# Kernel tuning notes

Measured on AMD Instinct MI355X. Metric: run time of the kernel, lower is better.

Reference implementation:

```python
import jax, jax.numpy as jnp
import numpy as np

jax.config.update("jax_enable_x64", True)  # original module is complex128/float64

UNITS = 256


def _logm(M):
    # Matrix log via eigendecomposition (jnp.linalg.eig is CPU-supported).
    # In the original TF graph logm feeds only the discarded _exp_tens list,
    # so no gradient ever flows through it; we mirror that with stop_gradient.
    w, V = jnp.linalg.eig(M)
    return (V * jnp.log(w)[None, :]) @ jnp.linalg.inv(V)


def setup_inputs() -> dict:
    key = jax.random.key(0)
    k = jax.random.split(key, 9)
    u = UNITS
    f64 = jnp.float64
    # real positive input so pow(x, units)/prod(x) is well-defined in float64
    x = jax.random.uniform(k[0], (u,), f64, 0.5, 1.5)
    A_r = jax.random.normal(k[1], (u,), f64)
    A_i = jax.random.normal(k[2], (u,), f64)
    cellA_r = jax.random.normal(k[3], (u,), f64)
    cellA_i = jax.random.normal(k[4], (u,), f64)
    # Exp_window initialized to identity in TF; perturb slightly for a nontrivial logm
    Exp_window_r = jnp.eye(u, dtype=f64) + 0.1 * jax.random.normal(k[5], (u, u), f64)
    Exp_window_i = 0.1 * jax.random.normal(k[6], (u, u), f64)
    unit_window_r = 0.01 * jax.random.normal(k[7], (u, u), f64)
    unit_window_i = 0.01 * jax.random.normal(k[8], (u, u), f64)
    return dict(x=x, A_r=A_r, A_i=A_i, cellA_r=cellA_r, cellA_i=cellA_i,
                Exp_window_r=Exp_window_r, Exp_window_i=Exp_window_i,
                unit_window_r=unit_window_r, unit_window_i=unit_window_i)


def reference(x, A_r, A_i, cellA_r, cellA_i,
              Exp_window_r, Exp_window_i, unit_window_r, unit_window_i):
    u = x.shape[0]
    A = A_r + 1j * A_i                       # MyRNN.A, [u]
    cellA = cellA_r + 1j * cellA_i           # MyRNNCell.A, [u]
    Ew = Exp_window_r + 1j * Exp_window_i    # [u, u]
    uw = unit_window_r + 1j * unit_window_i  # [u, u]

    # --- generate_unitary ---
    dy = jnp.concatenate([jnp.zeros((1,), x.dtype), x[1:] - x[:-1]])
    cpx = jnp.exp(1j * dy)                                     # cos(dy)+i sin(dy)
    div = jnp.power(x, u) / jnp.prod(x)
    unit = cpx * jnp.power(div, 1.0 / u).astype(cpx.dtype)     # [u] complex128

    # --- FFT normalization ---
    ufft = jnp.fft.fft(unit)
    ufft = ufft / jnp.sum(ufft)

    # --- steady-state branch: batched expm of per-unit skew matrices ---
    L = jax.lax.stop_gradient(_logm(Ew))       # dead-end in original graph
    C = jnp.conj(L)                            # [u, u]
    M = ufft[:, None, None] * C[None]          # [u, u, u]
    skew = M - jnp.transpose(M, (0, 2, 1))     # skew-symmetrized per unit
    exp_tens = jax.vmap(jax.scipy.linalg.expm)(skew)  # [u, u, u] complex128

    # --- cell: elementwise unitary update ---
    cell = jnp.conj(cellA) * (A * unit)        # [u]

    # --- rolling window state updates (training=True, counter >= units) ---
    log_diff = jnp.log(cell) - jnp.log(unit)
    new_uw = jnp.roll(uw, 1, axis=0).at[0].set(log_diff)
    new_Ew = jnp.conj(Ew) @ jax.scipy.linalg.expm(new_uw)

    # --- output ---
    update = x + jnp.angle(cell)               # [u] float64
    return (update, exp_tens, new_uw, new_Ew)
```

## Files before the change

### kernel.cpp

```cpp
#include <hip/hip_runtime.h>
#include <hip/hip_bf16.h>
#include <math.h>

#define NN 65536
#define MATD 131072L
#define MAT0 32768L

#define SC_DT 0
#define SC_NUINV 3
#define SC_EXPM_S 4
#define SC_EXPM_SCALE 5
#define SC_NORMS2 6
#define SC_MU 7
#define W_UNIT_RE 64
#define W_UNIT_IM 320
#define W_C_RE 576
#define W_C_IM 832
#define W_LD_RE 1088
#define W_LD_IM 1344
#define W_SU 1600
#define W_SLOT 1856
#define W_SLOTU 2112
#define W_W 2432
#define BARB 19456
#define BARM 23552
#define TRBASE 24064
#define NRM_ROW 31872
#define NRM_COL 32128
#define NRM_DEV 32384
#define NPOOL 256

#define S_EW 0
#define S_NUW 1
#define S_LAT 2
#define S_T2 3
#define S_T3 4
#define S_T4 5
#define S_E1 6
#define S_E2 7
#define S_M 8
#define S_M2 9
#define S_Y 10
#define S_Y2 11
#define S_IY 12
#define S_X 13
#define S_X2 14
#define S_T 15
#define S_W 16
#define S_V 17
#define S_G 18
#define S_G2 19
#define PBASE 20
#define POOL0 52

#define PI_D 3.14159265358979323846
#define LOG_SCALE 32.0

__device__ inline double ldin(const void* p, int i, int dt){
    if (dt == 0) return (double)__bfloat162float(((const __hip_bfloat16*)p)[i]);
    if (dt == 1) return (double)((const float*)p)[i];
    return ((const double*)p)[i];
}

__global__ __launch_bounds__(256) void k_init(double* ws){
    ws[blockIdx.x * 256 + threadIdx.x] = 0.0;
}

__global__ __launch_bounds__(64) void k_detect(const void* x, double* ws){
    __shared__ int ok[3];
    int t = threadIdx.x;
    if (t < 3) ok[t] = 1;
    __syncthreads();
    const __hip_bfloat16* pb = (const __hip_bfloat16*)x;
    for (int k = t; k < 256; k += 64){
        float v = __bfloat162float(pb[k]);
        if (!(v > 0.40f && v < 1.60f)) ok[0] = 0;
    }
    const float* pf = (const float*)x;
    { float v = pf[t]; if (!(v > 0.40f && v < 1.60f)) ok[1] = 0; }
    const double* pd = (const double*)x;
    { double v = pd[t]; if (!(v > 0.40 && v < 1.60)) ok[2] = 0; }
    __syncthreads();
    if (t == 0) ws[SC_DT] = ok[0] ? 0.0 : (ok[1] ? 1.0 : 2.0);
}

__global__ __launch_bounds__(256) void k_small(
    const void* xin, const void* Ar, const void* Ai,
    const void* cAr, const void* cAi,
    double* ws, float* out)
{
    __shared__ double xs[256], twc[256], tws[256], ur[256], ui[256], red[256];
    int t = threadIdx.x;
    int dt = (int)ws[SC_DT];
    double x = ldin(xin, t, dt);
    xs[t] = x;
    red[t] = log(x);
    double ang = -2.0 * PI_D * (double)t / 256.0;
    twc[t] = cos(ang); tws[t] = sin(ang);
    __syncthreads();
    for (int s = 128; s > 0; s >>= 1){ if (t < s) red[t] += red[t+s]; __syncthreads(); }
    double slog = red[0];
    __syncthreads();
    double dy = (t == 0) ? 0.0 : (x - xs[t-1]);
    double r = x * exp(-slog / 256.0);
    double unr = r * cos(dy), uni = r * sin(dy);
    ur[t] = unr; ui[t] = uni;
    ws[W_UNIT_RE + t] = unr; ws[W_UNIT_IM + t] = uni;
    __syncthreads();
    double fr = 0.0, fi = 0.0;
    for (int n = 0; n < 256; n++){
        int m = (t * n) & 255;
        double c = twc[m], s = tws[m];
        fr += ur[n]*c - ui[n]*s;
        fi += ur[n]*s + ui[n]*c;
    }
    red[t] = fr; __syncthreads();
    for (int s = 128; s > 0; s >>= 1){ if (t < s) red[t] += red[t+s]; __syncthreads(); }
    double sr = red[0]; __syncthreads();
    red[t] = fi; __syncthreads();
    for (int s = 128; s > 0; s >>= 1){ if (t < s) red[t] += red[t+s]; __syncthreads(); }
    double si = red[0];
    double den = sr*sr + si*si;
    double cr = (fr*sr + fi*si) / den, ci = (fi*sr - fr*si) / den;
    ws[W_C_RE + t] = cr; ws[W_C_IM + t] = ci;
    double ar = ldin(Ar, t, dt), ai = ldin(Ai, t, dt);
    double car = ldin(cAr, t, dt), cai = ldin(cAi, t, dt);
    double pr = ar*unr - ai*uni, pi = ar*uni + ai*unr;
    double qr = car*pr + cai*pi, qi = car*pi - cai*pr;
    out[t] = (float)(x + atan2(qi, qr));
    double ldr = 0.5 * log((qr*qr + qi*qi) / (unr*unr + uni*uni));
    double ldi = atan2(qi, qr) - atan2(uni, unr);
    ws[W_LD_RE + t] = ldr; ws[W_LD_IM + t] = ldi;
}

__global__ __launch_bounds__(256) void k_build_mats(
    const void* Ewr, const void* Ewi, const void* uwr, const void* uwi, double* ws)
{
    int ij = blockIdx.x * 256 + threadIdx.x;
    int i = ij >> 8, j = ij & 255;
    int dt = (int)ws[SC_DT];
    double* EW = ws + MAT0 + (size_t)S_EW * MATD;
    EW[ij] = ldin(Ewr, ij, dt); EW[NN + ij] = ldin(Ewi, ij, dt);
    double* U = ws + MAT0 + (size_t)S_NUW * MATD;
    if (i == 0){ U[ij] = ws[W_LD_RE + j]; U[NN + ij] = ws[W_LD_IM + j]; }
    else { int src = (i-1)*256 + j; U[ij] = ldin(uwr, src, dt); U[NN + ij] = ldin(uwi, src, dt); }
}

__global__ __launch_bounds__(256) void k_norm1inf(const double* M, double* ws, int idx)
{
    __shared__ double cs[256], rs[256];
    int t = threadIdx.x;
    double c = 0.0, r = 0.0;
    for (int i = 0; i < 256; i++){
        c += fabs(M[i*256 + t]) + fabs(M[NN + i*256 + t]);
        r += fabs(M[t*256 + i]) + fabs(M[NN + t*256 + i]);
    }
    cs[t] = c; rs[t] = r; __syncthreads();
    for (int s = 128; s > 0; s >>= 1){
        if (t < s){ cs[t] = fmax(cs[t], cs[t+s]); rs[t] = fmax(rs[t], rs[t+s]); }
        __syncthreads();
    }
    if (t == 0){
        ws[idx] = cs[0]; ws[idx+1] = rs[0];
        ws[SC_NUINV] = 1.0 / (cs[0] * rs[0]);
    }
}

__global__ __launch_bounds__(256) void k_fro(const double* M, double* ws)
{
    __shared__ double red[256];
    int t = threadIdx.x;
    double s = 0.0;
    for (int i = 0; i < 256; i++){
        double a = M[i*256 + t], b = M[NN + i*256 + t];
        s += a*a + b*b;
    }
    red[t] = s; __syncthreads();
    for (int k = 128; k > 0; k >>= 1){ if (t < k) red[t] += red[t+k]; __syncthreads(); }
    if (t == 0) ws[14] = red[0];
}

__global__ void k_snorm(double* ws)
{
    double b1 = sqrt(ws[12] * ws[13]);
    double b2 = sqrt(ws[14]);
    ws[SC_NORMS2] = fmin(b1, b2);
}

__global__ __launch_bounds__(256) void k_zgemm(
    const double* __restrict__ Ab, const double* __restrict__ Bb,
    double* __restrict__ Cb, const double* __restrict__ Db,
    int preA, int preB, double alpha, double beta, double gamma,
    double* __restrict__ ws, int fm, int round, int flagIdx, int trIdx,
    long sA, long sB, long sC)
{
    int z = blockIdx.z;
    const double* A = Ab + (size_t)z * sA;
    const double* B = Bb + (size_t)z * sB;
    double* C = Cb + (size_t)z * sC;
    int tx = threadIdx.x & 15, ty = threadIdx.x >> 4;
    int row = blockIdx.y * 16 + ty, col = blockIdx.x * 16 + tx;
    if (fm == 1 && round > (int)ws[SC_EXPM_S]){
        C[row*256 + col] = A[row*256 + col];
        C[NN + row*256 + col] = A[NN + row*256 + col];
        return;
    }
    __shared__ double Asr[16][17], Asi[16][17], Bsr[16][17], Bsi[16][17];
    double cr = 0.0, ci = 0.0;
    for (int k0 = 0; k0 < 256; k0 += 16){
        int ac = k0 + tx;
        double a_re = A[row*256 + ac], a_im = A[NN + row*256 + ac];
        if (preA == 1) a_im = -a_im;
        else if (preA == 2){ if (row == ac) a_re -= 1.0; }
        int br = k0 + ty;
        double b_re = B[br*256 + col], b_im = B[NN + br*256 + col];
        if (preB == 1){ b_re = ((br == col) ? 2.0 : 0.0) - b_re; b_im = -b_im; }
        Asr[ty][tx] = a_re; Asi[ty][tx] = a_im;
        Bsr[ty][tx] = b_re; Bsi[ty][tx] = b_im;
        __syncthreads();
        #pragma unroll
        for (int kk = 0; kk < 16; kk++){
            double xr = Asr[ty][kk], xi = Asi[ty][kk];
            double yr = Bsr[kk][tx], yi = Bsi[kk][tx];
            cr += xr*yr - xi*yi;
            ci += xr*yi + xi*yr;
        }
        __syncthreads();
    }
    double outr = alpha * cr, outi = alpha * ci;
    if (Db){ outr += beta * Db[row*256 + col]; outi += beta * Db[NN + row*256 + col]; }
    if (row == col) outr += gamma;
    C[row*256 + col] = outr;
    C[NN + row*256 + col] = outi;
}

__global__ __launch_bounds__(256) void k_combine(double* ws, int dst,
    int s1, int s2, int s3, int s4,
    double a1, double a2, double a3, double a4, double g, int mode)
{
    int ij = blockIdx.x * 256 + threadIdx.x;
    int i = ij >> 8, j = ij & 255;
    double f1 = 1.0, f2 = 1.0;
    if (mode == 1){ f1 = ws[SC_EXPM_SCALE]; }
    double* C = ws + MAT0 + (size_t)dst * MATD;
    double r = 0.0, m = 0.0;
    if (s1 >= 0){ const double* X = ws + MAT0 + (size_t)s1 * MATD; r += a1*f1*X[ij]; m += a1*f1*X[NN+ij]; }
    if (s2 >= 0){ const double* X = ws + MAT0 + (size_t)s2 * MATD; r += a2*f2*X[ij]; m += a2*f2*X[NN+ij]; }
    if (s3 >= 0){ const double* X = ws + MAT0 + (size_t)s3 * MATD; r += a3*X[ij]; m += a3*X[NN+ij]; }
    if (s4 >= 0){ const double* X = ws + MAT0 + (size_t)s4 * MATD; r += a4*X[ij]; m += a4*X[NN+ij]; }
    if (i == j) r += g;
    C[ij] = r; C[NN + ij] = m;
}

__global__ void k_expm_prep(double* ws)
{
    if (threadIdx.x == 0 && blockIdx.x == 0){
        double n1 = ws[8];
        int s = 0;
        if (n1 > 0.5){
            s = (int)ceil(log2(n1 / 0.5));
            if (s < 0) s = 0; if (s > 10) s = 10;
        }
        ws[SC_EXPM_S] = (double)s;
        ws[SC_EXPM_SCALE] = ldexp(1.0, -s);
    }
}

struct ShMemC {
    double Ar[2][16][17], Ai[2][16][17], Br[2][16][17], Bi[2][16][17];
    double redB[256];
    double trR[16], trI[16];
};

struct GOp {
    const double* A; const double* B; double* C;
    double sA, dA, sB, dB;
    double alpha, beta;
    const double* D; double sD, dD;
    double gamma;
    double* tr;
};

struct Ctx {
    double* ws; ShMemC* sh;
    unsigned int bgen;
    int t, b, team, tt, tx, ty, bx, by, row, col, ij2, pl, li, lj, tr_idx;
    bool diagre;

    __device__ void init(double* ws_, ShMemC* sh_){
        ws = ws_; sh = sh_;
        t = threadIdx.x; b = blockIdx.x;
        team = t >> 8; tt = t & 255;
        tx = tt & 15; ty = tt >> 4;
        bx = b & 15; by = b >> 4;
        row = by*16 + ty; col = bx*16 + tx;
        ij2 = b*512 + t;
        pl = ij2 >> 16;
        int lin = ij2 & 65535;
        li = lin >> 8; lj = lin & 255;
        tr_idx = (lj << 8) + li + (pl ? NN : 0);
        diagre = (pl == 0) && (li == lj);
        bgen = __hip_atomic_load((unsigned int*)(ws + BARB + 16), __ATOMIC_RELAXED,
                                 __HIP_MEMORY_SCOPE_AGENT);
    }
    __device__ double* SL(int s){ return ws + MAT0 + (size_t)s * MATD; }

    __device__ void spinwait(unsigned int* gline, unsigned int g){
        while (__hip_atomic_load(gline, __ATOMIC_RELAXED,
                                 __HIP_MEMORY_SCOPE_AGENT) == g)
            __builtin_amdgcn_s_sleep(2);
        if (__hip_atomic_load(gline, __ATOMIC_ACQUIRE,
                              __HIP_MEMORY_SCOPE_AGENT) == g)
            __builtin_amdgcn_s_sleep(1);
    }

    __device__ void GS(){
        __syncthreads();
        if (t == 0){
            unsigned int g = bgen;
            int grp = b & 7;
            unsigned int* aline  = (unsigned int*)(ws + BARB + grp*512);
            unsigned int* gline  = (unsigned int*)(ws + BARB + grp*512 + 16);
            unsigned int* master = (unsigned int*)(ws + BARM);
            unsigned int a = __hip_atomic_fetch_add(aline, 1u, __ATOMIC_ACQ_REL,
                                                    __HIP_MEMORY_SCOPE_AGENT);
            if (a == 31u){
                unsigned int m = __hip_atomic_fetch_add(master, 1u, __ATOMIC_ACQ_REL,
                                                        __HIP_MEMORY_SCOPE_AGENT);
                if (m == 7u){
                    __hip_atomic_store(master, 0u, __ATOMIC_RELAXED, __HIP_MEMORY_SCOPE_AGENT);
                    for (int q = 0; q < 8; q++)
                        __hip_atomic_store((unsigned int*)(ws + BARB + q*512), 0u,
                                           __ATOMIC_RELAXED, __HIP_MEMORY_SCOPE_AGENT);
                    for (int q = 0; q < 8; q++)
                        __hip_atomic_store((unsigned int*)(ws + BARB + q*512 + 16), g + 1u,
                                           __ATOMIC_RELEASE, __HIP_MEMORY_SCOPE_AGENT);
                } else spinwait(gline, g);
            } else spinwait(gline, g);
        }
        __syncthreads();
        bgen++;
    }

    __device__ double bmax(int base){
        double v = ws[base + (t & 255)];
        #pragma unroll
        for (int m = 32; m >= 1; m >>= 1) v = fmax(v, __shfl_xor(v, m));
        if ((t & 63) == 0) sh->redB[t >> 6] = v;
        __syncthreads();
        double u = sh->redB[0];
        #pragma unroll
        for (int q = 1; q < 8; q++) u = fmax(u, sh->redB[q]);
        __syncthreads();
        return u;
    }

    __device__ void partials(const double* M, bool withDev){
        double v, dv = 0.0;
        if (t < 256){
            double e = M[b*256 + t], f2 = M[NN + b*256 + t];
            v = fabs(e) + fabs(f2);
            if (withDev) dv = fabs(e - ((b == t) ? 1.0 : 0.0)) + fabs(f2);
        } else {
            int c2 = t - 256;
            v = fabs(M[c2*256 + b]) + fabs(M[NN + c2*256 + b]);
        }
        #pragma unroll
        for (int m = 32; m >= 1; m >>= 1){ v += __shfl_xor(v, m); dv += __shfl_xor(dv, m); }
        if ((t & 63) == 0){ sh->redB[t >> 6] = v; sh->redB[8 + (t >> 6)] = dv; }
        __syncthreads();
        if (t == 0){
            ws[NRM_ROW + b] = sh->redB[0] + sh->redB[1] + sh->redB[2] + sh->redB[3];
            if (withDev)
                ws[NRM_DEV + b] = sh->redB[8] + sh->redB[9] + sh->redB[10] + sh->redB[11];
        }
        if (t == 256){
            ws[NRM_COL + b] = sh->redB[4] + sh->redB[5] + sh->redB[6] + sh->redB[7];
        }
        __syncthreads();
    }

    __device__ void gemm(const double* A, const double* B, double* C,
                         double sA, double dA, double sB, double dB,
                         double alpha, double beta, const double* D,
                         double sD, double dD, double gamma, double* tr){
        double lar[8], lai[8], lbr[8], lbi[8];
        const double* Arow = A + (size_t)row*256;
        const double* Bcol = B + col;
        #pragma unroll
        for (int s = 0; s < 8; s++){
            int kb = (team << 7) + (s << 4);
            lar[s] = Arow[kb + tx];
            lai[s] = Arow[NN + kb + tx];
            lbr[s] = Bcol[(size_t)(kb + ty)*256];
            lbi[s] = Bcol[(size_t)NN + (size_t)(kb + ty)*256];
        }
        {
            double dm = 0.0;
            #pragma unroll
            for (int s = 0; s < 8; s++) dm += lar[s] + lai[s] + lbr[s] + lbi[s];
            asm volatile("" :: "v"(dm));
        }
        double cr = 0.0, ci = 0.0;
        #pragma unroll
        for (int s = 0; s < 8; s++){
            int kb = (team << 7) + (s << 4);
            int ac = kb + tx, brx = kb + ty;
            sh->Ar[team][ty][tx] = sA * lar[s] + ((row == ac) ? dA : 0.0);
            sh->Ai[team][ty][tx] = sA * lai[s];
            sh->Br[team][ty][tx] = sB * lbr[s] + ((brx == col) ? dB : 0.0);
            sh->Bi[team][ty][tx] = sB * lbi[s];
            __syncthreads();
            #pragma unroll
            for (int kk = 0; kk < 16; kk++){
                double xr = sh->Ar[team][ty][kk], xi = sh->Ai[team][ty][kk];
                double yr = sh->Br[team][kk][tx], yi = sh->Bi[team][kk][tx];
                cr += xr*yr - xi*yi;
                ci += xr*yi + xi*yr;
            }
            __syncthreads();
        }
        if (team == 1){ sh->Ar[1][ty][tx] = cr; sh->Ai[1][ty][tx] = ci; }
        __syncthreads();
        if (team == 0){
            cr += sh->Ar[1][ty][tx]; ci += sh->Ai[1][ty][tx];
            cr *= alpha; ci *= alpha;
            if (D){
                cr += beta * (sD * D[row*256 + col] + ((row == col) ? dD : 0.0));
                ci += beta * (sD * D[NN + row*256 + col]);
            }
            if (row == col) cr += gamma;
            C[row*256 + col] = cr;
            C[NN + row*256 + col] = ci;
        }
        if (tr && bx == by){
            if (team == 0 && ty == tx){ sh->trR[ty] = cr; sh->trI[ty] = ci; }
            __syncthreads();
            if (t == 0){
                double sr = 0.0, si = 0.0;
                for (int q = 0; q < 16; q++){ sr += sh->trR[q]; si += sh->trI[q]; }
                atomicAdd(tr, sr); atomicAdd(tr + 1, si);
            }
        }
        __syncthreads();
    }

    __device__ void gemm2(const GOp& o0, const GOp& o1){
        const GOp& d = team ? o1 : o0;
        double lar[16], lai[16], lbr[16], lbi[16];
        const double* Arow = d.A + (size_t)row*256;
        const double* Bcol = d.B + col;
        #pragma unroll
        for (int s = 0; s < 16; s++){
            int kb = s << 4;
            lar[s] = Arow[kb + tx];
            lai[s] = Arow[NN + kb + tx];
            lbr[s] = Bcol[(size_t)(kb + ty)*256];
            lbi[s] = Bcol[(size_t)NN + (size_t)(kb + ty)*256];
        }
        {
            double dm = 0.0;
            #pragma unroll
            for (int s = 0; s < 16; s++) dm += lar[s] + lai[s] + lbr[s] + lbi[s];
            asm volatile("" :: "v"(dm));
        }
        double cr = 0.0, ci = 0.0;
        #pragma unroll
        for (int s = 0; s < 16; s++){
            int kb = s << 4;
            int ac = kb + tx, brx = kb + ty;
            sh->Ar[team][ty][tx] = d.sA * lar[s] + ((row == ac) ? d.dA : 0.0);
            sh->Ai[team][ty][tx] = d.sA * lai[s];
            sh->Br[team][ty][tx] = d.sB * lbr[s] + ((brx == col) ? d.dB : 0.0);
            sh->Bi[team][ty][tx] = d.sB * lbi[s];
            __syncthreads();
            #pragma unroll
            for (int kk = 0; kk < 16; kk++){
                double xr = sh->Ar[team][ty][kk], xi = sh->Ai[team][ty][kk];
                double yr = sh->Br[team][kk][tx], yi = sh->Bi[team][kk][tx];
                cr += xr*yr - xi*yi;
                ci += xr*yi + xi*yr;
            }
            __syncthreads();
        }
        cr *= d.alpha; ci *= d.alpha;
        if (d.D){
            cr += d.beta * (d.sD * d.D[row*256 + col] + ((row == col) ? d.dD : 0.0));
            ci += d.beta * (d.sD * d.D[NN + row*256 + col]);
        }
        if (row == col) cr += d.gamma;
        d.C[row*256 + col] = cr;
        d.C[NN + row*256 + col] = ci;
        if (o0.tr && bx == by){
            if (team == 0 && ty == tx){ sh->trR[ty] = cr; sh->trI[ty] = ci; }
            __syncthreads();
            if (t == 0){
                double sr = 0.0, si = 0.0;
                for (int q = 0; q < 16; q++){ sr += sh->trR[q]; si += sh->trI[q]; }
                atomicAdd(o0.tr, sr); atomicAdd(o0.tr + 1, si);
            }
        }
        __syncthreads();
    }

    __device__ double* inv(const double* A, double dev, int maxit, int mode,
                           int invid, double& n1, double& ninf){
        double* X  = SL(S_X);  double* X2 = SL(S_X2);
        double* R  = SL(S_T);  double* R2 = SL(S_IY);
        n1 = bmax(NRM_COL); ninf = bmax(NRM_ROW);
        bool scaled = false; double a = 1e-7;
        bool virt = false;
        double* trb = ws + TRBASE + (size_t)invid * 128;
        if (mode == 0){
            if (dev < 0.95){
                virt = true;
                gemm(A, A, R, 1,0, -1,2, -1.0, 0.0, nullptr, 0,0, 1.0, trb);
            } else {
                scaled = true;
                double al = 1.0 / (n1 * ninf);
                double v = A[tr_idx] * al;
                X[ij2] = pl ? -v : v;
                GS();
                gemm(A, X, R, 1,0, 1,0, -1.0, 0.0, nullptr, 0,0, 1.0, trb);
            }
        } else {
            gemm(A, X, R, 1,0, 1,0, -1.0, 0.0, nullptr, 0,0, 1.0, trb);
        }
        GS();
        double* xc = X; double* xo = X2; double* rc = R; double* ro = R2;
        bool canFall = (mode == 2);
        for (int i = 0; i < maxit; i++){
            if (t == 0){ sh->trR[0] = trb[2*i]; sh->trI[0] = trb[2*i+1]; }
            __syncthreads();
            double resid = fabs(sh->trR[0]) + fabs(sh->trI[0]);
            __syncthreads();
            if (resid < 1e-5){
                if (virt){
                    double v = -A[ij2];
                    if (diagre) v += 2.0;
                    xc[ij2] = v;
                    GS();
                }
                break;
            }
            if (canFall && i >= 4 && resid > 1e4){
                canFall = false; scaled = true; a = 1e-7;
                double al = 1.0 / (n1 * ninf);
                double v = A[tr_idx] * al;
                xo[ij2] = pl ? -v : v;
                GS();
                gemm(A, xo, ro, 1,0, 1,0, -1.0, 0.0, nullptr, 0,0, 1.0, trb + 2*(i+1));
                GS();
                double* tm = xc; xc = xo; xo = tm;
                tm = rc; rc = ro; ro = tm;
                continue;
            }
            double xi_ = 1.0;
            if (scaled){
                if (a > 0.5) scaled = false;
                else { xi_ = 2.0/(1.0 + a); double o = 1.0 + a; a = 4.0*a/(o*o); }
            }
            double omx = 1.0 - xi_;
            GOp oR = { rc, rc, ro, xi_, omx, xi_, omx, 1.0, 0.0, nullptr, 0,0, 0.0,
                       trb + 2*(i+1) };
            GOp oX;
            if (virt){
                oX = GOp{ A, rc, xo, -1.0, 2.0, 1,0, xi_*xi_, xi_*(2.0 - xi_),
                          A, -1.0, 2.0, 0.0, nullptr };
                virt = false;
            } else {
                oX = GOp{ xc, rc, xo, 1,0, 1,0, xi_*xi_, xi_*(2.0 - xi_),
                          xc, 1.0, 0.0, 0.0, nullptr };
            }
            gemm2(oR, oX);
            GS();
            double* tm = xc; xc = xo; xo = tm;
            tm = rc; rc = ro; ro = tm;
        }
        return xc;
    }
};

__global__ __launch_bounds__(512, 1) void k_logm_db(double* __restrict__ ws, int invBase)
{
    __shared__ ShMemC sh;
    Ctx c; c.init(ws, &sh);
    double* dMm = c.SL(S_M);  double* dM2 = c.SL(S_M2);
    double* dYy = c.SL(S_Y);  double* dY2 = c.SL(S_Y2);
    double* dG  = c.SL(S_G);
    double* EW  = c.SL(S_EW);
    const int ij2 = c.ij2;

    dMm[ij2] = EW[ij2];
    dYy[ij2] = EW[ij2];
    c.partials(EW, true);
    c.GS();
    double* mc = dMm; double* mo = dM2; double* yc = dYy; double* yo = dY2;
    double dev = c.bmax(NRM_DEV);
    int invid = invBase;
    for (int it = 0; it < 20; it++){
        if (dev < 1e-7) break;
        double nm1, nminf;
        double* iy = c.inv(mc, dev, 40, 0, invid++, nm1, nminf);
        c.gemm(yc, iy, dG, 1,0, 1,0, 1.0, 0.0, nullptr, 0,0, 0.0, nullptr);
        c.partials(iy, false);
        c.GS();
        double ni1 = c.bmax(NRM_COL), niinf = c.bmax(NRM_ROW);
        double mu = pow((ni1 * niinf) / (nm1 * nminf), 0.125);
        if (!(mu > 0.125)) mu = 0.125;
        if (mu > 8.0) mu = 8.0;
        double mu2 = mu*mu, rmu = 1.0/mu, rmu2 = rmu*rmu;
        {
            double r = 0.25 * (mu2 * mc[ij2] + rmu2 * iy[ij2]);
            if (c.diagre) r += 0.5;
            mo[ij2] = r;
            yo[ij2] = 0.5 * (mu * yc[ij2] + rmu * dG[ij2]);
        }
        c.GS();
        c.partials(mo, true);
        c.GS();
        dev = c.bmax(NRM_DEV);
        double* tm = mc; mc = mo; mo = tm;
        tm = yc; yc = yo; yo = tm;
    }
    EW[ij2] = yc[ij2];
}

__global__ __launch_bounds__(512, 1) void k_logm_sq(double* __restrict__ ws)
{
    __shared__ ShMemC sh;
    Ctx c; c.init(ws, &sh);
    double* dYy = c.SL(S_Y);  double* dY2 = c.SL(S_Y2);
    double* dX  = c.SL(S_X);  double* dX2 = c.SL(S_X2);
    double* dT  = c.SL(S_T);
    double* EW  = c.SL(S_EW);
    const int ij2 = c.ij2;

    c.partials(EW, false);
    c.GS();
    double cc = sqrt(c.bmax(NRM_COL) * c.bmax(NRM_ROW));
    double invc = 1.0 / cc, sc = sqrt(cc);
    dYy[ij2] = EW[ij2] * invc;
    dX[ij2]  = c.diagre ? 1.0 : 0.0;
    c.GS();
    double* Ycur = dYy; double* Yalt = dY2;
    double* Zcur = dX;  double* Zalt = dX2;
    for (int it = 0; it < 30; it++){
        c.gemm(Zcur, Ycur, dT, 1,0, 1,0, 1.0, 0.0, nullptr, 0,0, 0.0, nullptr);
        c.GS();
        c.partials(dT, true);
        c.GS();
        double dv = c.bmax(NRM_DEV);
        if (dv < 1e-11) break;
        GOp oY = { Ycur, dT, Yalt, 1,0, -1.0,3.0, 0.5, 0.0, nullptr, 0,0, 0.0, nullptr };
        GOp oZ = { dT, Zcur, Zalt, -1.0,3.0, 1,0, 0.5, 0.0, nullptr, 0,0, 0.0, nullptr };
        c.gemm2(oY, oZ);
        c.GS();
        double* tm = Ycur; Ycur = Yalt; Yalt = tm;
        tm = Zcur; Zcur = Zalt; Zalt = tm;
    }
    EW[ij2] = sc * Ycur[ij2];
}

__global__ __launch_bounds__(512, 1) void k_logm_cay(double* __restrict__ ws, int invBase)
{
    __shared__ ShMemC sh;
    Ctx c; c.init(ws, &sh);
    double* dX  = c.SL(S_X);
    double* dG  = c.SL(S_G);  double* dG2 = c.SL(S_G2);
    double* dW  = c.SL(S_W);  double* dV  = c.SL(S_V);
    double* dLT = c.SL(S_LAT);
    double* dS  = c.SL(PBASE);
    double* EW  = c.SL(S_EW);
    const int ij2 = c.ij2;

    dG[ij2] = EW[ij2] + (c.diagre ? 1.0 : 0.0);
    dX[ij2] = -0.25 * EW[ij2] + (c.diagre ? 0.75 : 0.0);
    c.GS();
    c.partials(dG, false);
    c.GS();
    double cn1, cninf;
    double* giy = c.inv(dG, 0.0, 40, 2, invBase, cn1, cninf);
    c.gemm(EW, giy, dW, 1,-1, 1,0, 1.0, 0.0, nullptr, 0,0, 0.0, nullptr);
    c.GS();
    c.gemm(dW, dW, dV, 1,0, 1,0, 1.0, 0.0, nullptr, 0,0, 0.0, nullptr);
    c.partials(dW, false);
    c.GS();
    double nW = c.bmax(NRM_ROW);
    double q = nW * nW;
    int J = 19;
    if (q < 0.5){
        J = 1;
        double qp = q * q;
        while (J < 19 && qp >= 1e-16 * (1.0 - q)){ qp *= q; J++; }
    }
    dG[ij2] = c.diagre ? 1.0/(double)(2*J + 1) : 0.0;
    c.GS();
    double* gc = dG; double* go = dG2;
    for (int j = J - 1; j >= 0; j--){
        c.gemm(dV, gc, go, 1,0, 1,0, 1.0, 0.0, nullptr, 0,0, 1.0/(double)(2*j + 1), nullptr);
        c.GS();
        double* tm = gc; gc = go; go = tm;
    }
    c.gemm(dW, gc, dLT, 1,0, 1,0, 1.0, 0.0, nullptr, 0,0, 0.0, nullptr);
    c.GS();
    double vv = dLT[ij2] - dLT[c.tr_idx];
    dS[ij2] = c.pl ? -LOG_SCALE * vv : LOG_SCALE * vv;
}

__global__ __launch_bounds__(256) void k_theta_pool(double* ws)
{
    __shared__ double th[256]; __shared__ int rk[256];
    int t = threadIdx.x;
    double nS = ws[SC_NORMS2];
    double cr = ws[W_C_RE + t], ci = ws[W_C_IM + t];
    th[t] = sqrt(cr*cr + ci*ci) * nS;
    __syncthreads();
    int r = 0;
    for (int v = 0; v < 256; v++){
        if (th[v] > th[t] || (th[v] == th[t] && v < t)) r++;
    }
    rk[t] = r;
    __syncthreads();
    if (t == 0){
        int cnt = 0;
        for (int u = 0; u < 256; u++){
            double s = 0.0; int slot = -1;
            if (th[u] > 4.0 && rk[u] < NPOOL){
                double e = ceil(log2(th[u] / 4.0));
                if (e < 1.0) e = 1.0; if (e > 12.0) e = 12.0;
                s = e; slot = cnt;
                ws[W_SLOTU + cnt] = (double)u;
                cnt++;
            }
            ws[W_SU + u] = s;
            ws[W_SLOT + u] = (double)slot;
        }
        for (int k = cnt; k < NPOOL; k++) ws[W_SLOTU + k] = -1.0;
    }
}

__global__ __launch_bounds__(256) void k_weights(double* ws)
{
    int u = threadIdx.x;
    double sc = ldexp(1.0, -(int)ws[W_SU + u]);
    double cr = ws[W_C_RE + u] * sc, ci = ws[W_C_IM + u] * sc;
    double wr = 1.0, wi = 0.0;
    ws[W_W + (u*33)*2] = 1.0; ws[W_W + (u*33)*2 + 1] = 0.0;
    for (int k = 1; k <= 32; k++){
        double inv = 1.0 / (double)k;
        double nr = (wr*cr - wi*ci) * inv, ni = (wr*ci + wi*cr) * inv;
        wr = nr; wi = ni;
        ws[W_W + (u*33 + k)*2] = wr;
        ws[W_W + (u*33 + k)*2 + 1] = wi;
    }
}

__global__ __launch_bounds__(256) void k_combo(double* ws, float* out, long off_ex, int f,
                                               int pass, int K)
{
    __shared__ double wre[16][33], wim[16][33];
    __shared__ int anywork;
    int t = threadIdx.x;
    int row = blockIdx.x, ug = blockIdx.y;
    if (t == 0) anywork = (pass == 0) ? 1 : 0;
    __syncthreads();
    if (pass > 0 && t < 16){
        int u = ug*16 + t;
        int slot = (int)ws[W_SLOT + u];
        int phys = slot - pass * K;
        if (slot >= 0 && phys >= 0 && phys < K) anywork = 1;
    }
    __syncthreads();
    if (!anywork) return;
    for (int i = t; i < 16*33; i += 256){
        int g = i / 33, k = i % 33;
        int u = ug*16 + g;
        wre[g][k] = ws[W_W + (u*33 + k)*2];
        wim[g][k] = ws[W_W + (u*33 + k)*2 + 1];
    }
    __syncthreads();
    int j = t, ij = row*256 + j;
    double ar[16], ai[16];
    #pragma unroll
    for (int g = 0; g < 16; g++){
        ar[g] = (row == j) ? wre[g][0] : 0.0;
        ai[g] = (row == j) ? wim[g][0] : 0.0;
    }
    for (int k = 1; k <= 32; k++){
        const double* SP = ws + MAT0 + (size_t)(PBASE + k - 1) * MATD;
        double sre = SP[ij], sim = SP[NN + ij];
        #pragma unroll
        for (int g = 0; g < 16; g++){
            ar[g] += wre[g][k]*sre - wim[g][k]*sim;
            ai[g] += wre[g][k]*sim + wim[g][k]*sre;
        }
    }
    for (int g = 0; g < 16; g++){
        int u = ug*16 + g;
        int slot = (int)ws[W_SLOT + u];
        if (slot >= 0){
            int phys = slot - pass * K;
            if (phys >= 0 && phys < K){
                double* P = ws + MAT0 + (size_t)(POOL0 + phys) * MATD;
                P[ij] = ar[g]; P[NN + ij] = ai[g];
            }
        } else if (pass == 0){
            long base = off_ex + (long)u * NN * f + (long)ij * f;
            out[base] = (float)ar[g];
            if (f == 2) out[base + 1] = (float)ai[g];
        }
    }
}

__global__ __launch_bounds__(256) void k_pool_sq(double* ws, int round, int pass, int K)
{
    int z = blockIdx.z;
    int vs = pass * K + z;
    int u = (vs < NPOOL) ? (int)ws[W_SLOTU + vs] : -1;
    if (u < 0) return;
    if (round > (int)ws[W_SU + u]) return;
    const double* A = ws + MAT0 + (size_t)(POOL0 + ((round & 1) ? 0 : K) + z) * MATD;
    double* C = ws + MAT0 + (size_t)(POOL0 + ((round & 1) ? K : 0) + z) * MATD;
    int tx = threadIdx.x & 15, ty = threadIdx.x >> 4;
    int row = blockIdx.y*16 + ty, col = blockIdx.x*16 + tx;
    __shared__ double Asr[16][17], Asi[16][17], Bsr[16][17], Bsi[16][17];
    double cr = 0.0, ci = 0.0;
    for (int k0 = 0; k0 < 256; k0 += 16){
        Asr[ty][tx] = A[row*256 + k0 + tx];
        Asi[ty][tx] = A[NN + row*256 + k0 + tx];
        Bsr[ty][tx] = A[(k0 + ty)*256 + col];
        Bsi[ty][tx] = A[NN + (k0 + ty)*256 + col];
        __syncthreads();
        #pragma unroll
        for (int kk = 0; kk < 16; kk++){
            double xr = Asr[ty][kk], xi = Asi[ty][kk];
            double yr = Bsr[kk][tx], yi = Bsi[kk][tx];
            cr += xr*yr - xi*yi;
            ci += xr*yi + xi*yr;
        }
        __syncthreads();
    }
    C[row*256 + col] = cr;
    C[NN + row*256 + col] = ci;
}

__global__ __launch_bounds__(256) void k_pool_out(const double* ws, float* out, long off_ex,
                                                  int f, int pass, int K)
{
    int z = blockIdx.y;
    int vs = pass * K + z;
    int u = (vs < NPOOL) ? (int)ws[W_SLOTU + vs] : -1;
    if (u < 0) return;
    int su = (int)ws[W_SU + u];
    int ij = blockIdx.x * 256 + threadIdx.x;
    const double* P = ws + MAT0 + (size_t)(POOL0 + ((su & 1) ? K : 0) + z) * MATD;
    long base = off_ex + (long)u * NN * f + (long)ij * f;
    out[base] = (float)P[ij];
    if (f == 2) out[base + 1] = (float)P[NN + ij];
}

__global__ __launch_bounds__(256) void k_cast_out(const double* ws, int slot, float* out, long off, int f)
{
    int ij = blockIdx.x * 256 + threadIdx.x;
    const double* P = ws + MAT0 + (size_t)slot * MATD;
    out[off + (long)ij * f] = (float)P[ij];
    if (f == 2) out[off + (long)ij * f + 1] = (float)P[NN + ij];
}

extern "C" void kernel_launch(void* const* d_in, const int* in_sizes, int n_in,
                              void* d_out, int out_size, void* d_ws, size_t ws_size,
                              hipStream_t stream)
{
    double* ws = (double*)d_ws;
    float* out = (float*)d_out;

    int f = (out_size >= 33816832) ? 2 : 1;
    long off_ex = 256;
    long off_uw = off_ex + (long)f * 16777216L;
    long off_ew = off_uw + (long)f * 65536L;

    k_init<<<128, 256, 0, stream>>>(ws);
    k_detect<<<1, 64, 0, stream>>>(d_in[0], ws);
    k_small<<<1, 256, 0, stream>>>(d_in[0], d_in[1], d_in[2], d_in[3], d_in[4], ws, out);

    long slotsAvail = (long)(ws_size / 8 - MAT0) / MATD;
    if (slotsAvail < POOL0 + 32) return;
    int K = (int)((slotsAvail - POOL0) / 2);
    if (K > NPOOL) K = NPOOL;
    if (K < 16) K = 16;
    int P = (NPOOL + K - 1) / K;

    auto MP = [&](int s){ return ws + MAT0 + (size_t)s * MATD; };
    auto ZG = [&](int a, int b, int c, int preA, int preB, double al, double be,
                  int d, double ga, int fm, int round){
        k_zgemm<<<dim3(16,16,1), 256, 0, stream>>>(MP(a), MP(b), MP(c),
            d >= 0 ? MP(d) : nullptr, preA, preB, al, be, ga, ws,
            fm, round, 0, 0, 0L, 0L, 0L);
    };
    auto GEMM = [&](int a, int b, int c, int preA, int preB, double al, double be, int d, double ga){
        ZG(a, b, c, preA, preB, al, be, d, ga, 0, 0);
    };

    k_build_mats<<<256, 256, 0, stream>>>(d_in[5], d_in[6], d_in[7], d_in[8], ws);
    k_cast_out<<<256, 256, 0, stream>>>(ws, S_NUW, out, off_uw, f);

    static const double INVF[17] = {
        1.0, 1.0, 0.5, 1.0/6.0, 1.0/24.0, 1.0/120.0, 1.0/720.0, 1.0/5040.0,
        1.0/40320.0, 1.0/362880.0, 1.0/3628800.0, 1.0/39916800.0, 1.0/479001600.0,
        1.0/6227020800.0, 1.0/87178291200.0, 1.0/1307674368000.0, 1.0/20922789888000.0 };
    k_norm1inf<<<1, 256, 0, stream>>>(MP(S_NUW), ws, 8);
    k_expm_prep<<<1, 64, 0, stream>>>(ws);
    k_combine<<<256, 256, 0, stream>>>(ws, S_LAT, S_NUW, -1, -1, -1, 1.0, 0, 0, 0, 0.0, 1);
    GEMM(S_LAT, S_LAT, S_T2, 0, 0, 1.0, 0.0, -1, 0.0);
    GEMM(S_T2, S_LAT, S_T3, 0, 0, 1.0, 0.0, -1, 0.0);
    GEMM(S_T2, S_T2, S_T4, 0, 0, 1.0, 0.0, -1, 0.0);
    k_combine<<<256, 256, 0, stream>>>(ws, S_E1, -1, -1, -1, -1, 0, 0, 0, 0, INVF[16], 0);
    for (int b = 3; b >= 0; b--){
        GEMM(S_T4, S_E1, S_E2, 0, 0, 1.0, 0.0, -1, 0.0);
        k_combine<<<256, 256, 0, stream>>>(ws, S_E1, S_E2, S_LAT, S_T2, S_T3,
            1.0, INVF[4*b+1], INVF[4*b+2], INVF[4*b+3], INVF[4*b], 0);
    }
    for (int r = 1; r <= 10; r++){
        int src = (r & 1) ? S_E1 : S_E2, dst = (r & 1) ? S_E2 : S_E1;
        ZG(src, src, dst, 0, 0, 1.0, 0.0, -1, 0.0, 1, r);
    }
    GEMM(S_EW, S_E1, S_M2, 1, 0, 1.0, 0.0, -1, 0.0);
    k_cast_out<<<256, 256, 0, stream>>>(ws, S_M2, out, off_ew, f);

    {
        int ib0 = 0, ib1 = 20, ib2 = 40;
        { void* a[] = { (void*)&ws, (void*)&ib0 };
          hipLaunchCooperativeKernel((void*)k_logm_db, dim3(256), dim3(512), a, 0, stream); }
        { void* a[] = { (void*)&ws, (void*)&ib1 };
          hipLaunchCooperativeKernel((void*)k_logm_db, dim3(256), dim3(512), a, 0, stream); }
        { void* a[] = { (void*)&ws };
          hipLaunchCooperativeKernel((void*)k_logm_sq, dim3(256), dim3(512), a, 0, stream); }
        { void* a[] = { (void*)&ws };
          hipLaunchCooperativeKernel((void*)k_logm_sq, dim3(256), dim3(512), a, 0, stream); }
        { void* a[] = { (void*)&ws, (void*)&ib2 };
          hipLaunchCooperativeKernel((void*)k_logm_cay, dim3(256), dim3(512), a, 0, stream); }
    }

    k_norm1inf<<<1, 256, 0, stream>>>(MP(PBASE), ws, 12);
    k_fro<<<1, 256, 0, stream>>>(MP(PBASE), ws);
    k_snorm<<<1, 1, 0, stream>>>(ws);
    k_theta_pool<<<1, 256, 0, stream>>>(ws);
    k_weights<<<1, 256, 0, stream>>>(ws);
    for (int m = 1; m < 32; m *= 2){
        int cnt = (m < 32 - m) ? m : (32 - m);
        k_zgemm<<<dim3(16,16,cnt), 256, 0, stream>>>(MP(PBASE + m - 1), MP(PBASE), MP(PBASE + m),
            nullptr, 0, 0, 1.0, 0.0, 0.0, ws, 0, 0, 0, 0, 0L, MATD, MATD);
    }
    for (int p = 0; p < P; p++){
        k_combo<<<dim3(256,16), 256, 0, stream>>>(ws, out, off_ex, f, p, K);
        for (int r = 1; r <= 12; r++)
            k_pool_sq<<<dim3(16,16,K), 256, 0, stream>>>(ws, r, p, K);
        k_pool_out<<<dim3(256,K), 256, 0, stream>>>(ws, out, off_ex, f, p, K);
    }
}
```

Before: 11.61 ms.

## Cut grid barriers by fusing norm reductions into GEMM and barrier payloads

Removes several grid-wide barriers per iteration in the logm Denman-Beavers, square-root and Cayley/inverse loops. It fuses the deviation-norm reduction into the GEMM epilogue with atomics into double-buffered accumulators, and folds the row/dev norms of the next iterate into the update step. The Newton-inverse residual trace is broadcast through the barrier release line as a payload instead of a separate shared-memory read. The DB scaling now uses only infinity norms (fourth root) instead of 1-norm times inf-norm, which changes the numerical scaling heuristic. Atomic float accumulation makes the reductions nondeterministic in order.

```diff
diff --git a/kernel.cpp b/kernel.cpp
--- a/kernel.cpp
+++ b/kernel.cpp
@@ -25,9 +25,13 @@
 #define BARB 19456
 #define BARM 23552
 #define TRBASE 24064
+#define B_INF0 29440
+#define B_INF1 29696
+#define B_DEV0 29952
+#define B_DEV1 30208
+#define XNRM 30720
 #define NRM_ROW 31872
 #define NRM_COL 32128
-#define NRM_DEV 32384
 #define NPOOL 256
 
 #define S_EW 0
@@ -270,6 +274,7 @@
     double Ar[2][16][17], Ai[2][16][17], Br[2][16][17], Bi[2][16][17];
     double redB[256];
     double trR[16], trI[16];
+    double pay0, pay1;
 };
 
 struct GOp {
@@ -314,7 +319,7 @@
             __builtin_amdgcn_s_sleep(1);
     }
 
-    __device__ void GS(){
+    __device__ void GS(const double* pay){
         __syncthreads();
         if (t == 0){
             unsigned int g = bgen;
@@ -322,6 +327,7 @@
             unsigned int* aline  = (unsigned int*)(ws + BARB + grp*512);
             unsigned int* gline  = (unsigned int*)(ws + BARB + grp*512 + 16);
             unsigned int* master = (unsigned int*)(ws + BARM);
+            double p0 = 0.0, p1 = 0.0;
             unsigned int a = __hip_atomic_fetch_add(aline, 1u, __ATOMIC_ACQ_REL,
                                                     __HIP_MEMORY_SCOPE_AGENT);
             if (a == 31u){
@@ -329,14 +335,27 @@
                                                         __HIP_MEMORY_SCOPE_AGENT);
                 if (m == 7u){
                     __hip_atomic_store(master, 0u, __ATOMIC_RELAXED, __HIP_MEMORY_SCOPE_AGENT);
-                    for (int q = 0; q < 8; q++)
+                    if (pay){ p0 = pay[0]; p1 = pay[1]; }
+                    for (int q = 0; q < 8; q++){
                         __hip_atomic_store((unsigned int*)(ws + BARB + q*512), 0u,
                                            __ATOMIC_RELAXED, __HIP_MEMORY_SCOPE_AGENT);
+                        if (pay){
+                            ws[BARB + q*512 + 17] = p0;
+                            ws[BARB + q*512 + 18] = p1;
+                        }
+                    }
                     for (int q = 0; q < 8; q++)
                         __hip_atomic_store((unsigned int*)(ws + BARB + q*512 + 16), g + 1u,
                                            __ATOMIC_RELEASE, __HIP_MEMORY_SCOPE_AGENT);
-                } else spinwait(gline, g);
-            } else spinwait(gline, g);
+                } else {
+                    spinwait(gline, g);
+                    if (pay){ p0 = ws[BARB + grp*512 + 17]; p1 = ws[BARB + grp*512 + 18]; }
+                }
+            } else {
+                spinwait(gline, g);
+                if (pay){ p0 = ws[BARB + grp*512 + 17]; p1 = ws[BARB + grp*512 + 18]; }
+            }
+            if (pay){ sh->pay0 = p0; sh->pay1 = p1; }
         }
         __syncthreads();
         bgen++;
@@ -355,13 +374,13 @@
         return u;
     }
 
-    __device__ void partials(const double* M, bool withDev){
-        double v, dv = 0.0;
+    __device__ void partials(const double* M, int rowDst, int colDst, int devDst){
+        double v = 0.0, dv = 0.0;
         if (t < 256){
             double e = M[b*256 + t], f2 = M[NN + b*256 + t];
             v = fabs(e) + fabs(f2);
-            if (withDev) dv = fabs(e - ((b == t) ? 1.0 : 0.0)) + fabs(f2);
-        } else {
+            if (devDst >= 0) dv = fabs(e - ((b == t) ? 1.0 : 0.0)) + fabs(f2);
+        } else if (colDst >= 0){
             int c2 = t - 256;
             v = fabs(M[c2*256 + b]) + fabs(M[NN + c2*256 + b]);
         }
@@ -370,12 +389,12 @@
         if ((t & 63) == 0){ sh->redB[t >> 6] = v; sh->redB[8 + (t >> 6)] = dv; }
         __syncthreads();
         if (t == 0){
-            ws[NRM_ROW + b] = sh->redB[0] + sh->redB[1] + sh->redB[2] + sh->redB[3];
-            if (withDev)
-                ws[NRM_DEV + b] = sh->redB[8] + sh->redB[9] + sh->redB[10] + sh->redB[11];
-        }
-        if (t == 256){
-            ws[NRM_COL + b] = sh->redB[4] + sh->redB[5] + sh->redB[6] + sh->redB[7];
+            ws[rowDst + b] = sh->redB[0] + sh->redB[1] + sh->redB[2] + sh->redB[3];
+            if (devDst >= 0)
+                ws[devDst + b] = sh->redB[8] + sh->redB[9] + sh->redB[10] + sh->redB[11];
+        }
+        if (t == 256 && colDst >= 0){
+            ws[colDst + b] = sh->redB[4] + sh->redB[5] + sh->redB[6] + sh->redB[7];
         }
         __syncthreads();
     }
@@ -383,7 +402,8 @@
     __device__ void gemm(const double* A, const double* B, double* C,
                          double sA, double dA, double sB, double dB,
                          double alpha, double beta, const double* D,
-                         double sD, double dD, double gamma, double* tr){
+                         double sD, double dD, double gamma, double* tr,
+                         double* devW, double* devZ){
         double lar[8], lai[8], lbr[8], lbi[8];
         const double* Arow = A + (size_t)row*256;
         const double* Bcol = B + col;
@@ -433,6 +453,14 @@
             C[row*256 + col] = cr;
             C[NN + row*256 + col] = ci;
         }
+        if (devW){
+            double v = 0.0;
+            if (team == 0) v = fabs(cr - ((row == col) ? 1.0 : 0.0)) + fabs(ci);
+            #pragma unroll
+            for (int m = 1; m < 16; m <<= 1) v += __shfl_xor(v, m);
+            if (team == 0 && tx == 0) atomicAdd(&devW[row], v);
+            if (team == 1 && tt < 16) devZ[by*16 + tt] = 0.0;
+        }
         if (tr && bx == by){
             if (team == 0 && ty == tx){ sh->trR[ty] = cr; sh->trI[ty] = ci; }
             __syncthreads();
@@ -503,43 +531,46 @@
         __syncthreads();
     }
 
-    __device__ double* inv(const double* A, double dev, int maxit, int mode,
-                           int invid, double& n1, double& ninf){
+    __device__ double* inv(const double* A, double dev, int maxit, int mode, int invid){
         double* X  = SL(S_X);  double* X2 = SL(S_X2);
         double* R  = SL(S_T);  double* R2 = SL(S_IY);
-        n1 = bmax(NRM_COL); ninf = bmax(NRM_ROW);
         bool scaled = false; double a = 1e-7;
         bool virt = false;
+        double n1 = 0.0, ninf = 0.0;
         double* trb = ws + TRBASE + (size_t)invid * 128;
         if (mode == 0){
             if (dev < 0.95){
                 virt = true;
-                gemm(A, A, R, 1,0, -1,2, -1.0, 0.0, nullptr, 0,0, 1.0, trb);
+                gemm(A, A, R, 1,0, -1,2, -1.0, 0.0, nullptr, 0,0, 1.0, trb,
+                     nullptr, nullptr);
             } else {
+                partials(A, NRM_ROW, NRM_COL, -1);
+                GS(nullptr);
+                n1 = bmax(NRM_COL); ninf = bmax(NRM_ROW);
                 scaled = true;
                 double al = 1.0 / (n1 * ninf);
                 double v = A[tr_idx] * al;
                 X[ij2] = pl ? -v : v;
-                GS();
-                gemm(A, X, R, 1,0, 1,0, -1.0, 0.0, nullptr, 0,0, 1.0, trb);
+                GS(nullptr);
+                gemm(A, X, R, 1,0, 1,0, -1.0, 0.0, nullptr, 0,0, 1.0, trb,
+                     nullptr, nullptr);
             }
         } else {
-            gemm(A, X, R, 1,0, 1,0, -1.0, 0.0, nullptr, 0,0, 1.0, trb);
-        }
-        GS();
+            n1 = bmax(NRM_COL); ninf = bmax(NRM_ROW);
+            gemm(A, X, R, 1,0, 1,0, -1.0, 0.0, nullptr, 0,0, 1.0, trb,
+                 nullptr, nullptr);
+        }
+        GS(trb);
+        double resid = fabs(sh->pay0) + fabs(sh->pay1);
         double* xc = X; double* xo = X2; double* rc = R; double* ro = R2;
         bool canFall = (mode == 2);
         for (int i = 0; i < maxit; i++){
-            if (t == 0){ sh->trR[0] = trb[2*i]; sh->trI[0] = trb[2*i+1]; }
-            __syncthreads();
-            double resid = fabs(sh->trR[0]) + fabs(sh->trI[0]);
-            __syncthreads();
             if (resid < 1e-5){
                 if (virt){
                     double v = -A[ij2];
                     if (diagre) v += 2.0;
                     xc[ij2] = v;
-                    GS();
+                    GS(nullptr);
                 }
                 break;
             }
@@ -548,9 +579,11 @@
                 double al = 1.0 / (n1 * ninf);
                 double v = A[tr_idx] * al;
                 xo[ij2] = pl ? -v : v;
-                GS();
-                gemm(A, xo, ro, 1,0, 1,0, -1.0, 0.0, nullptr, 0,0, 1.0, trb + 2*(i+1));
-                GS();
+                GS(nullptr);
+                gemm(A, xo, ro, 1,0, 1,0, -1.0, 0.0, nullptr, 0,0, 1.0,
+                     trb + 2*(i+1), nullptr, nullptr);
+                GS(trb + 2*(i+1));
+                resid = fabs(sh->pay0) + fabs(sh->pay1);
                 double* tm = xc; xc = xo; xo = tm;
                 tm = rc; rc = ro; ro = tm;
                 continue;
@@ -573,7 +606,8 @@
                           xc, 1.0, 0.0, 0.0, nullptr };
             }
             gemm2(oR, oX);
-            GS();
+            GS(trb + 2*(i+1));
+            resid = fabs(sh->pay0) + fabs(sh->pay1);
             double* tm = xc; xc = xo; xo = tm;
             tm = rc; rc = ro; ro = tm;
         }
@@ -593,33 +627,57 @@
 
     dMm[ij2] = EW[ij2];
     dYy[ij2] = EW[ij2];
-    c.partials(EW, true);
-    c.GS();
+    c.partials(EW, B_INF0, -1, B_DEV0);
+    if (c.t == 0){ ws[B_INF1 + c.b] = 0.0; ws[B_DEV1 + c.b] = 0.0; }
+    c.GS(nullptr);
     double* mc = dMm; double* mo = dM2; double* yc = dYy; double* yo = dY2;
-    double dev = c.bmax(NRM_DEV);
+    int cur = 0;
+    double dev = c.bmax(B_DEV0);
+    double nm  = c.bmax(B_INF0);
     int invid = invBase;
     for (int it = 0; it < 20; it++){
         if (dev < 1e-7) break;
-        double nm1, nminf;
-        double* iy = c.inv(mc, dev, 40, 0, invid++, nm1, nminf);
-        c.gemm(yc, iy, dG, 1,0, 1,0, 1.0, 0.0, nullptr, 0,0, 0.0, nullptr);
-        c.partials(iy, false);
-        c.GS();
-        double ni1 = c.bmax(NRM_COL), niinf = c.bmax(NRM_ROW);
-        double mu = pow((ni1 * niinf) / (nm1 * nminf), 0.125);
+        double* iy = c.inv(mc, dev, 40, 0, invid++);
+        c.gemm(yc, iy, dG, 1,0, 1,0, 1.0, 0.0, nullptr, 0,0, 0.0, nullptr,
+               nullptr, nullptr);
+        c.partials(iy, XNRM, -1, -1);
+        c.GS(nullptr);
+        double niinf = c.bmax(XNRM);
+        double mu = pow(niinf / nm, 0.25);
         if (!(mu > 0.125)) mu = 0.125;
         if (mu > 8.0) mu = 8.0;
         double mu2 = mu*mu, rmu = 1.0/mu, rmu2 = rmu*rmu;
+        int nxt = cur ^ 1;
         {
             double r = 0.25 * (mu2 * mc[ij2] + rmu2 * iy[ij2]);
             if (c.diagre) r += 0.5;
             mo[ij2] = r;
             yo[ij2] = 0.5 * (mu * yc[ij2] + rmu * dG[ij2]);
-        }
-        c.GS();
-        c.partials(mo, true);
-        c.GS();
-        dev = c.bmax(NRM_DEV);
+            double av = fabs(r);
+            double dvv = fabs(r - (c.diagre ? 1.0 : 0.0));
+            #pragma unroll
+            for (int m = 32; m >= 1; m >>= 1){ av += __shfl_xor(av, m); dvv += __shfl_xor(dvv, m); }
+            int w = c.t >> 6;
+            if ((c.t & 63) == 0){ sh.redB[w] = dvv; sh.redB[16 + w] = av; }
+            __syncthreads();
+            int DEVn = nxt ? B_DEV1 : B_DEV0, INFn = nxt ? B_INF1 : B_INF0;
+            int DEVc = cur ? B_DEV1 : B_DEV0, INFc = cur ? B_INF1 : B_INF0;
+            int r0 = ((c.b & 127) << 1);
+            if (c.t == 0){
+                atomicAdd(&ws[DEVn + r0], sh.redB[0]+sh.redB[1]+sh.redB[2]+sh.redB[3]);
+                atomicAdd(&ws[INFn + r0], sh.redB[16]+sh.redB[17]+sh.redB[18]+sh.redB[19]);
+                if (c.b < 128){ ws[DEVc + r0] = 0.0; ws[INFc + r0] = 0.0; }
+            }
+            if (c.t == 256){
+                atomicAdd(&ws[DEVn + r0+1], sh.redB[4]+sh.redB[5]+sh.redB[6]+sh.redB[7]);
+                atomicAdd(&ws[INFn + r0+1], sh.redB[20]+sh.redB[21]+sh.redB[22]+sh.redB[23]);
+                if (c.b < 128){ ws[DEVc + r0+1] = 0.0; ws[INFc + r0+1] = 0.0; }
+            }
+        }
+        c.GS(nullptr);
+        cur = nxt;
+        dev = c.bmax(cur ? B_DEV1 : B_DEV0);
+        nm  = c.bmax(cur ? B_INF1 : B_INF0);
         double* tm = mc; mc = mo; mo = tm;
         tm = yc; yc = yo; yo = tm;
     }
@@ -636,26 +694,29 @@
     double* EW  = c.SL(S_EW);
     const int ij2 = c.ij2;
 
-    c.partials(EW, false);
-    c.GS();
+    c.partials(EW, NRM_ROW, NRM_COL, -1);
+    if (c.t == 0){ ws[B_DEV0 + c.b] = 0.0; ws[B_DEV1 + c.b] = 0.0; }
+    c.GS(nullptr);
     double cc = sqrt(c.bmax(NRM_COL) * c.bmax(NRM_ROW));
     double invc = 1.0 / cc, sc = sqrt(cc);
     dYy[ij2] = EW[ij2] * invc;
     dX[ij2]  = c.diagre ? 1.0 : 0.0;
-    c.GS();
+    c.GS(nullptr);
     double* Ycur = dYy; double* Yalt = dY2;
     double* Zcur = dX;  double* Zalt = dX2;
     for (int it = 0; it < 30; it++){
-        c.gemm(Zcur, Ycur, dT, 1,0, 1,0, 1.0, 0.0, nullptr, 0,0, 0.0, nullptr);
-        c.GS();
-        c.partials(dT, true);
-        c.GS();
-        double dv = c.bmax(NRM_DEV);
+        int wr = it & 1;
+        double* devW = ws + (wr ? B_DEV1 : B_DEV0);
+        double* devZ = ws + (wr ? B_DEV0 : B_DEV1);
+        c.gemm(Zcur, Ycur, dT, 1,0, 1,0, 1.0, 0.0, nullptr, 0,0, 0.0, nullptr,
+               devW, devZ);
+        c.GS(nullptr);
+        double dv = c.bmax(wr ? B_DEV1 : B_DEV0);
         if (dv < 1e-11) break;
         GOp oY = { Ycur, dT, Yalt, 1,0, -1.0,3.0, 0.5, 0.0, nullptr, 0,0, 0.0, nullptr };
         GOp oZ = { dT, Zcur, Zalt, -1.0,3.0, 1,0, 0.5, 0.0, nullptr, 0,0, 0.0, nullptr };
         c.gemm2(oY, oZ);
-        c.GS();
+        c.GS(nullptr);
         double* tm = Ycur; Ycur = Yalt; Yalt = tm;
         tm = Zcur; Zcur = Zalt; Zalt = tm;
     }
@@ -676,16 +737,17 @@
 
     dG[ij2] = EW[ij2] + (c.diagre ? 1.0 : 0.0);
     dX[ij2] = -0.25 * EW[ij2] + (c.diagre ? 0.75 : 0.0);
-    c.GS();
-    c.partials(dG, false);
-    c.GS();
-    double cn1, cninf;
-    double* giy = c.inv(dG, 0.0, 40, 2, invBase, cn1, cninf);
-    c.gemm(EW, giy, dW, 1,-1, 1,0, 1.0, 0.0, nullptr, 0,0, 0.0, nullptr);
-    c.GS();
-    c.gemm(dW, dW, dV, 1,0, 1,0, 1.0, 0.0, nullptr, 0,0, 0.0, nullptr);
-    c.partials(dW, false);
-    c.GS();
+    c.GS(nullptr);
+    c.partials(dG, NRM_ROW, NRM_COL, -1);
+    c.GS(nullptr);
+    double* giy = c.inv(dG, 0.0, 40, 2, invBase);
+    c.gemm(EW, giy, dW, 1,-1, 1,0, 1.0, 0.0, nullptr, 0,0, 0.0, nullptr,
+           nullptr, nullptr);
+    c.GS(nullptr);
+    c.gemm(dW, dW, dV, 1,0, 1,0, 1.0, 0.0, nullptr, 0,0, 0.0, nullptr,
+           nullptr, nullptr);
+    c.partials(dW, NRM_ROW, -1, -1);
+    c.GS(nullptr);
     double nW = c.bmax(NRM_ROW);
     double q = nW * nW;
     int J = 19;
@@ -695,15 +757,17 @@
         while (J < 19 && qp >= 1e-16 * (1.0 - q)){ qp *= q; J++; }
     }
     dG[ij2] = c.diagre ? 1.0/(double)(2*J + 1) : 0.0;
-    c.GS();
+    c.GS(nullptr);
     double* gc = dG; double* go = dG2;
     for (int j = J - 1; j >= 0; j--){
-        c.gemm(dV, gc, go, 1,0, 1,0, 1.0, 0.0, nullptr, 0,0, 1.0/(double)(2*j + 1), nullptr);
-        c.GS();
+        c.gemm(dV, gc, go, 1,0, 1,0, 1.0, 0.0, nullptr, 0,0, 1.0/(double)(2*j + 1),
+               nullptr, nullptr, nullptr);
+        c.GS(nullptr);
         double* tm = gc; gc = go; go = tm;
     }
-    c.gemm(dW, gc, dLT, 1,0, 1,0, 1.0, 0.0, nullptr, 0,0, 0.0, nullptr);
-    c.GS();
+    c.gemm(dW, gc, dLT, 1,0, 1,0, 1.0, 0.0, nullptr, 0,0, 0.0, nullptr,
+           nullptr, nullptr);
+    c.GS(nullptr);
     double vv = dLT[ij2] - dLT[c.tr_idx];
     dS[ij2] = c.pl ? -LOG_SCALE * vv : LOG_SCALE * vv;
 }
```

Result: no change. 11.60 ms (-0.0%).
